# Kernel tuning notes

Hardware: AMD Instinct MI355X
Metric: run time of the kernel (lower is better)

Reference implementation:

```python
import jax, jax.numpy as jnp
import numpy as np

MAX_NODES = 32767   # complete binary tree, depth 15 (2**15 - 1)
N_FEATURES = 256
N_ACTIONS = 64
BATCH = 262144


def _build_tree(key):
    """Valid complete binary tree: internal node i has children 2i+1, 2i+2; leaves -1/-1."""
    idx = np.arange(MAX_NODES)
    left = 2 * idx + 1
    right = 2 * idx + 2
    internal = right < MAX_NODES
    children_left = np.where(internal, left, -1).astype(np.int32)
    children_right = np.where(internal, right, -1).astype(np.int32)
    k1, k2 = jax.random.split(key)
    features = jax.random.randint(k1, (MAX_NODES,), 0, N_FEATURES, dtype=jnp.int32)
    thresholds = jax.random.normal(k2, (MAX_NODES,), dtype=jnp.float32)
    return features, thresholds, jnp.asarray(children_left), jnp.asarray(children_right)


def setup_inputs() -> dict:
    key = jax.random.key(0)
    k_obs, k_tree, k_leaf = jax.random.split(key, 3)
    features, thresholds, children_left, children_right = _build_tree(k_tree)
    obs = jax.random.normal(k_obs, (BATCH, N_FEATURES), dtype=jnp.float32)
    leaf_logits = jax.random.normal(k_leaf, (MAX_NODES, N_ACTIONS), dtype=jnp.float32)
    return {
        "obs": obs,
        "features": features,
        "thresholds": thresholds,
        "children_left": children_left,
        "children_right": children_right,
        "leaf_logits": leaf_logits,
    }


def reference(obs, features, thresholds, children_left, children_right, leaf_logits):
    # Faithful translation of the flax module's while_loop tree traversal,
    # vmapped over a batch of observations.
    def traverse(o):  # o: [n_features]
        def cond(node_id):
            return children_left[node_id] != children_right[node_id]

        def body(node_id):
            go_left = o[features[node_id]] <= thresholds[node_id]
            return jax.lax.select(go_left, children_left[node_id], children_right[node_id])

        return jax.lax.while_loop(cond, body, jnp.int32(0))

    leaf_ids = jax.vmap(traverse)(obs)          # [B] int32
    return leaf_logits[leaf_ids]                # [B, n_actions]
```

## Files before the change

### kernel.cpp

```cpp
#include <hip/hip_runtime.h>


#define N_INTERN  16383
#define N_FEAT    256
#define N_ACT     64
#define BATCH     262144
#define BLOCK     512
#define GRID      256
#define ROWS_PB   (BATCH / GRID)
#define HROWS     32
#define HALVES    (ROWS_PB / HROWS)
#define DEPTH     14

typedef float f32x4 __attribute__((ext_vector_type(4)));
typedef __attribute__((address_space(3))) void        lds_void_t;
typedef const __attribute__((address_space(1))) void  glob_cvoid_t;

__device__ __forceinline__ void gload16(const void* g, void* l) {
    __builtin_amdgcn_global_load_lds((glob_cvoid_t*)g, (lds_void_t*)l, 16, 0, 0);
}

__global__ __launch_bounds__(BLOCK, 1) void tree_policy_kernel(
    const float* __restrict__ obs,
    const int*   __restrict__ features,
    const float* __restrict__ thresholds,
    const float* __restrict__ leaf_logits,
    float*       __restrict__ out)
{
    __shared__ float         sthr [N_INTERN];
    __shared__ unsigned char sfeat[N_INTERN];
    __shared__ __align__(16) float buf[2][HROWS * N_FEAT];

    const int tid  = threadIdx.x;
    const int lane = tid & 63;
    const int wave = tid >> 6;
    const long rowBase = (long)blockIdx.x * ROWS_PB;

    for (int i = tid; i < N_INTERN; i += BLOCK) {
        sthr[i]  = thresholds[i];
        sfeat[i] = (unsigned char)features[i];
    }
    const float thr_root  = thresholds[0];
    const int   feat_root = features[0];

    const int myrow_id = (wave << 2) | (lane >> 4);
    const int chunk    = lane & 15;

    auto dma = [&](int h) {
        const float* g = obs + (rowBase + (long)h * HROWS + (wave << 2)) * N_FEAT + lane * 4;
        char* l = (char*)&buf[h & 1][(wave << 2) * N_FEAT];
#pragma unroll
        for (int k = 0; k < 4; ++k)
            gload16(g + k * N_FEAT, l + k * 1024);
    };

    auto traverse = [&](int h) -> int {
        const float* myrow = &buf[h & 1][myrow_id * N_FEAT];
        int node = 0; float tcur = thr_root; int fcur = feat_root;
#pragma unroll
        for (int d = 0; d < DEPTH - 1; ++d) {
            const float x   = myrow[fcur];
            const int   c   = 2 * node + 1;
            const float tl  = sthr[c];
            const float trr = sthr[c + 1];
            const int   fl  = sfeat[c];
            const int   fr  = sfeat[c + 1];
            const bool  L   = (x <= tcur);
            node = L ? c : c + 1;
            tcur = L ? tl : trr;
            fcur = L ? fl : fr;
        }
        const float x = myrow[fcur];
        return 2 * node + ((x <= tcur) ? 1 : 2);
    };

    dma(0);
    asm volatile("s_waitcnt vmcnt(0) lgkmcnt(0)" ::: "memory");
    __builtin_amdgcn_s_barrier();

    dma(1);
    __builtin_amdgcn_sched_barrier(0);
    int node_prev = traverse(0);

    for (int h = 1; h < HALVES; ++h) {
        if (h == 1) asm volatile("s_waitcnt vmcnt(0)" ::: "memory");
        else        asm volatile("s_waitcnt vmcnt(1)" ::: "memory");
        __builtin_amdgcn_sched_barrier(0);
        const f32x4 v = *(const f32x4*)(leaf_logits + (size_t)node_prev * N_ACT + chunk * 4);
        __builtin_amdgcn_sched_barrier(0);
        if (h + 1 < HALVES) {
            dma(h + 1);
            __builtin_amdgcn_sched_barrier(0);
        }
        const long orow = rowBase + (long)(h - 1) * HROWS + myrow_id;
        __builtin_nontemporal_store(v, (f32x4*)(out + orow * N_ACT + chunk * 4));
        __builtin_amdgcn_sched_barrier(0);
        node_prev = traverse(h);
    }

    const f32x4 v = *(const f32x4*)(leaf_logits + (size_t)node_prev * N_ACT + chunk * 4);
    const long orow = rowBase + (long)(HALVES - 1) * HROWS + myrow_id;
    __builtin_nontemporal_store(v, (f32x4*)(out + orow * N_ACT + chunk * 4));
}

extern "C" void kernel_launch(void* const* d_in, const int* in_sizes, int n_in,
                              void* d_out, int out_size, void* d_ws, size_t ws_size,
                              hipStream_t stream) {
    const float* obs         = (const float*)d_in[0];
    const int*   features    = (const int*)  d_in[1];
    const float* thresholds  = (const float*)d_in[2];
    const float* leaf_logits = (const float*)d_in[5];
    float*       out         = (float*)d_out;

    tree_policy_kernel<<<dim3(GRID), dim3(BLOCK), 0, stream>>>(
        obs, features, thresholds, leaf_logits, out);
}
```

Baseline: 62.44 us.

## Prefetch obs into registers four groups ahead and deepen leaf-gather pipeline

Replaces the global-to-LDS direct loads with nontemporal register loads issued four row-groups ahead, which are then written into a double-buffered LDS tile before traversal. The leaf-logit gather is also pushed one stage deeper so that its latency overlaps with an additional traversal. The aim is to hide DRAM latency for obs and the logits gather behind more in-flight work. In exchange it uses more VGPRs for the four register prefetch groups, drops the explicit vmcnt waits, and relies on a single barrier when reusing the LDS buffer, which could leave a cross-wave race between writing a buffer and other waves still reading it.

```diff
diff --git a/kernel.cpp b/kernel.cpp
--- a/kernel.cpp
+++ b/kernel.cpp
@@ -13,12 +13,6 @@
 #define DEPTH     14
 
 typedef float f32x4 __attribute__((ext_vector_type(4)));
-typedef __attribute__((address_space(3))) void        lds_void_t;
-typedef const __attribute__((address_space(1))) void  glob_cvoid_t;
-
-__device__ __forceinline__ void gload16(const void* g, void* l) {
-    __builtin_amdgcn_global_load_lds((glob_cvoid_t*)g, (lds_void_t*)l, 16, 0, 0);
-}
 
 __global__ __launch_bounds__(BLOCK, 1) void tree_policy_kernel(
     const float* __restrict__ obs,
@@ -29,7 +23,7 @@
 {
     __shared__ float         sthr [N_INTERN];
     __shared__ unsigned char sfeat[N_INTERN];
-    __shared__ __align__(16) float buf[2][HROWS * N_FEAT];
+    __shared__ __align__(16) f32x4 buf[2][HROWS * N_FEAT / 4];
 
     const int tid  = threadIdx.x;
     const int lane = tid & 63;
@@ -46,16 +40,24 @@
     const int myrow_id = (wave << 2) | (lane >> 4);
     const int chunk    = lane & 15;
 
-    auto dma = [&](int h) {
-        const float* g = obs + (rowBase + (long)h * HROWS + (wave << 2)) * N_FEAT + lane * 4;
-        char* l = (char*)&buf[h & 1][(wave << 2) * N_FEAT];
+    const f32x4* gsrc = (const f32x4*)obs;
+    auto ldgrp = [&](int h, f32x4 (&pf)[4]) {
 #pragma unroll
-        for (int k = 0; k < 4; ++k)
-            gload16(g + k * N_FEAT, l + k * 1024);
+        for (int k = 0; k < 4; ++k) {
+            const long row = rowBase + (long)h * HROWS + (wave << 2) + k;
+            pf[k] = __builtin_nontemporal_load(&gsrc[row * 64 + lane]);
+        }
     };
 
+    f32x4 pfA[4], pfB[4], pfC[4], pfD[4];
+    ldgrp(0, pfA); ldgrp(1, pfB); ldgrp(2, pfC); ldgrp(3, pfD);
+
+    asm volatile("s_waitcnt lgkmcnt(0)" ::: "memory");
+    __builtin_amdgcn_s_barrier();
+    __builtin_amdgcn_sched_barrier(0);
+
     auto traverse = [&](int h) -> int {
-        const float* myrow = &buf[h & 1][myrow_id * N_FEAT];
+        const float* myrow = (const float*)&buf[h & 1][myrow_id * 64];
         int node = 0; float tcur = thr_root; int fcur = feat_root;
 #pragma unroll
         for (int d = 0; d < DEPTH - 1; ++d) {
@@ -74,33 +76,46 @@
         return 2 * node + ((x <= tcur) ? 1 : 2);
     };
 
-    dma(0);
-    asm volatile("s_waitcnt vmcnt(0) lgkmcnt(0)" ::: "memory");
-    __builtin_amdgcn_s_barrier();
+    int   n1 = 0, n2 = 0;
+    f32x4 v_old = {0.f, 0.f, 0.f, 0.f};
 
-    dma(1);
-    __builtin_amdgcn_sched_barrier(0);
-    int node_prev = traverse(0);
+    auto body = [&](int h, f32x4 (&pf)[4]) {
+        f32x4 v_new = v_old;
+        if (h >= 2)
+            v_new = *(const f32x4*)(leaf_logits + (size_t)n2 * N_ACT + chunk * 4);
+        __builtin_amdgcn_sched_barrier(0);
+        if (h >= 3) {
+            const long orow = rowBase + (long)(h - 3) * HROWS + myrow_id;
+            __builtin_nontemporal_store(v_old, (f32x4*)(out + orow * N_ACT + chunk * 4));
+        }
+        __builtin_amdgcn_sched_barrier(0);
+#pragma unroll
+        for (int k = 0; k < 4; ++k)
+            buf[h & 1][((wave << 2) + k) * 64 + lane] = pf[k];
+        if (h + 4 < HALVES) ldgrp(h + 4, pf);
+        __builtin_amdgcn_sched_barrier(0);
+        const int nd = traverse(h);
+        n2 = n1; n1 = nd;
+        v_old = v_new;
+    };
 
-    for (int h = 1; h < HALVES; ++h) {
-        if (h == 1) asm volatile("s_waitcnt vmcnt(0)" ::: "memory");
-        else        asm volatile("s_waitcnt vmcnt(1)" ::: "memory");
-        __builtin_amdgcn_sched_barrier(0);
-        const f32x4 v = *(const f32x4*)(leaf_logits + (size_t)node_prev * N_ACT + chunk * 4);
-        __builtin_amdgcn_sched_barrier(0);
-        if (h + 1 < HALVES) {
-            dma(h + 1);
-            __builtin_amdgcn_sched_barrier(0);
-        }
-        const long orow = rowBase + (long)(h - 1) * HROWS + myrow_id;
-        __builtin_nontemporal_store(v, (f32x4*)(out + orow * N_ACT + chunk * 4));
-        __builtin_amdgcn_sched_barrier(0);
-        node_prev = traverse(h);
+    for (int hh = 0; hh < HALVES; hh += 4) {
+        body(hh + 0, pfA);
+        body(hh + 1, pfB);
+        body(hh + 2, pfC);
+        body(hh + 3, pfD);
     }
 
-    const f32x4 v = *(const f32x4*)(leaf_logits + (size_t)node_prev * N_ACT + chunk * 4);
-    const long orow = rowBase + (long)(HALVES - 1) * HROWS + myrow_id;
-    __builtin_nontemporal_store(v, (f32x4*)(out + orow * N_ACT + chunk * 4));
+    {
+        const long o29 = rowBase + 29L * HROWS + myrow_id;
+        __builtin_nontemporal_store(v_old, (f32x4*)(out + o29 * N_ACT + chunk * 4));
+        const f32x4 v30 = *(const f32x4*)(leaf_logits + (size_t)n2 * N_ACT + chunk * 4);
+        const long o30 = rowBase + 30L * HROWS + myrow_id;
+        __builtin_nontemporal_store(v30, (f32x4*)(out + o30 * N_ACT + chunk * 4));
+        const f32x4 v31 = *(const f32x4*)(leaf_logits + (size_t)n1 * N_ACT + chunk * 4);
+        const long o31 = rowBase + 31L * HROWS + myrow_id;
+        __builtin_nontemporal_store(v31, (f32x4*)(out + o31 * N_ACT + chunk * 4));
+    }
 }
 
 extern "C" void kernel_launch(void* const* d_in, const int* in_sizes, int n_in,
```

Result: slower. 63.81 us (+2.2%).
